# Optimization experiments

Hardware: AMD Instinct MI355X
Metric: run time of the kernel (lower is better)

The kernel has to match this reference:

```python
import jax, jax.numpy as jnp
import numpy as np

EPS = 1e-5
H = 1024  # hidden_size
IN = 1024  # input_size
B = 4096


def _layer_norm(x, gamma, beta):
    mu = jnp.mean(x, axis=-1, keepdims=True)
    var = jnp.mean(jnp.square(x - mu), axis=-1, keepdims=True)
    return (x - mu) * jax.lax.rsqrt(var + EPS) * gamma + beta


def setup_inputs() -> dict:
    key = jax.random.key(0)
    ks = jax.random.split(key, 8)
    s_h = 1.0 / np.sqrt(H)
    s_x = 1.0 / np.sqrt(IN)
    return {
        "x": jax.random.normal(ks[0], (B, IN), dtype=jnp.float32),
        "h": jax.random.normal(ks[1], (B, H), dtype=jnp.float32),
        "c": jax.random.normal(ks[2], (B, H), dtype=jnp.float32),
        # hidden_lin: Linear(H, 4H) with bias; input_lin: Linear(IN, 4H) no bias
        "W_h": jax.random.uniform(ks[3], (H, 4 * H), jnp.float32, -s_h, s_h),
        "b_h": jax.random.uniform(ks[4], (4 * H,), jnp.float32, -s_h, s_h),
        "W_x": jax.random.uniform(ks[5], (IN, 4 * H), jnp.float32, -s_x, s_x),
        # 4 gate LayerNorms stacked [4,H], plus LayerNorm for c
        "ln_g": jnp.ones((4, H), jnp.float32),
        "ln_b": jnp.zeros((4, H), jnp.float32),
        "lnc_g": jnp.ones((H,), jnp.float32),
        "lnc_b": jnp.zeros((H,), jnp.float32),
    }


def reference(x, h, c, W_h, b_h, W_x, ln_g, ln_b, lnc_g, lnc_b):
    # ifgo = hidden_lin(h) + input_lin(x) : [B, 4H]
    ifgo = h @ W_h + b_h + x @ W_x
    ifgo = ifgo.reshape(x.shape[0], 4, H)  # [B, 4, H]
    ifgo = _layer_norm(ifgo, ln_g, ln_b)   # per-gate LayerNorm over last dim
    i, f, g, o = ifgo[:, 0], ifgo[:, 1], ifgo[:, 2], ifgo[:, 3]
    c_next = jax.nn.sigmoid(f) * c + jax.nn.sigmoid(i) * jnp.tanh(g)
    h_next = jax.nn.sigmoid(o) * jnp.tanh(_layer_norm(c_next, lnc_g, lnc_b))
    return (h_next, c_next)
```

## Files before the change

kernel.cpp:

```cpp
#include <hip/hip_runtime.h>

typedef short bf16x8 __attribute__((ext_vector_type(8)));
typedef unsigned short u16x8 __attribute__((ext_vector_type(8)));
typedef float f32x4  __attribute__((ext_vector_type(4)));

__device__ __forceinline__ float bf2f(unsigned short u) {
  union { unsigned int i; float f; } x; x.i = ((unsigned int)u) << 16; return x.f;
}
__device__ __forceinline__ unsigned short f2bf(float f) {
  union { float f; unsigned int i; } x; x.f = f;
  unsigned int r = x.i + 0x7fffu + ((x.i >> 16) & 1u);
  return (unsigned short)(r >> 16);
}
__device__ __forceinline__ float sigm(float v) { return 1.f / (1.f + __expf(-v)); }
__device__ __forceinline__ float tanh_(float v) { return 1.f - 2.f / (__expf(2.f * v) + 1.f); }
__device__ __forceinline__ int is_fp32(const void* lng) {
  return ((*(const unsigned int*)lng) & 0xFFFFu) == 0u;
}

#define AS1 __attribute__((address_space(1)))
#define AS3 __attribute__((address_space(3)))

__global__ __launch_bounds__(256) void prep_kernel(
    const void* __restrict__ h, const void* __restrict__ x,
    const void* __restrict__ Wh, const void* __restrict__ Wx,
    const void* __restrict__ lng,
    unsigned short* __restrict__ Ap, unsigned short* __restrict__ Wt)
{
  __shared__ __align__(16) unsigned short tkn[64][64];
  const int fp = is_fp32(lng);
  if (blockIdx.x < 4096) {
    const int row = blockIdx.x;
    const int col = threadIdx.x * 8;
    const void* src; int sc;
    if (col < 1024) { src = h; sc = col; } else { src = x; sc = col - 1024; }
    u16x8 o;
    if (fp) {
      const float* s = (const float*)src + (size_t)row * 1024 + sc;
      float4 a = *(const float4*)s;
      float4 b = *(const float4*)(s + 4);
      o[0] = f2bf(a.x); o[1] = f2bf(a.y); o[2] = f2bf(a.z); o[3] = f2bf(a.w);
      o[4] = f2bf(b.x); o[5] = f2bf(b.y); o[6] = f2bf(b.z); o[7] = f2bf(b.w);
    } else {
      o = *(const u16x8*)((const unsigned short*)src + (size_t)row * 1024 + sc);
    }
    *(u16x8*)(Ap + (size_t)row * 2048 + col) = o;
  } else {
    const int bid = blockIdx.x - 4096;
    const int n0 = (bid & 63) * 64;
    const int k0 = (bid >> 6) * 64;
    const int t = threadIdx.x;
    const void* src; int krow;
    if (k0 < 1024) { src = Wh; krow = k0; } else { src = Wx; krow = k0 - 1024; }
    if (fp) {
#pragma unroll
      for (int i = 0; i < 4; ++i) {
        const int k  = (t >> 4) + i * 16;
        const int n4 = (t & 15) * 4;
        float4 w = *(const float4*)((const float*)src + (size_t)(krow + k) * 4096 + n0 + n4);
        ushort4 u; u.x = f2bf(w.x); u.y = f2bf(w.y); u.z = f2bf(w.z); u.w = f2bf(w.w);
        *(ushort4*)&tkn[k][n4] = u;
      }
    } else {
#pragma unroll
      for (int i = 0; i < 2; ++i) {
        const int k  = (t >> 3) + i * 32;
        const int n8 = (t & 7) * 8;
        *(u16x8*)&tkn[k][n8] =
            *(const u16x8*)((const unsigned short*)src + (size_t)(krow + k) * 4096 + n0 + n8);
      }
    }
    __syncthreads();
#pragma unroll
    for (int i = 0; i < 2; ++i) {
      const int n  = (t >> 3) + i * 32;
      const int k8 = (t & 7) * 8;
      u16x8 o;
#pragma unroll
      for (int j = 0; j < 8; ++j) o[j] = tkn[k8 + j][n];
      *(u16x8*)(Wt + (size_t)(n0 + n) * 2048 + k0 + k8) = o;
    }
  }
}


#define BAR()   __builtin_amdgcn_s_barrier()
#define VMW(N)  { asm volatile("s_waitcnt vmcnt(" #N ")" ::: "memory"); }
#define LGKM0() { asm volatile("s_waitcnt lgkmcnt(0)" ::: "memory"); }

#define LOAD_A(DB, MH)                                                         \
  { const unsigned short* _ba = &As[DB][(MH)*128 + wr*64 + fr][0];             \
    _Pragma("unroll") for (int mi = 0; mi < 4; ++mi)                           \
      _Pragma("unroll") for (int kh = 0; kh < 2; ++kh)                         \
        a[mi][kh] = *(const bf16x8*)(_ba + mi*1024 + ((kh*4 + fq) ^ xk) * 8); }

#define LOAD_B(DB, NH, BT)                                                     \
  { const unsigned short* _bb = &Bs[DB][(NH)*128 + wc*32 + fr][0];             \
    _Pragma("unroll") for (int ni = 0; ni < 2; ++ni)                           \
      _Pragma("unroll") for (int kh = 0; kh < 2; ++kh)                         \
        (BT)[ni][kh] = *(const bf16x8*)(_bb + ni*1024 + ((kh*4 + fq) ^ xk) * 8); }

#define MFMA16(MH, NH, BT)                                                     \
  { __builtin_amdgcn_s_setprio(1);                                             \
    _Pragma("unroll") for (int kh = 0; kh < 2; ++kh)                           \
      _Pragma("unroll") for (int mi = 0; mi < 4; ++mi)                         \
        _Pragma("unroll") for (int ni = 0; ni < 2; ++ni)                       \
          acc[MH][mi][NH][ni] = __builtin_amdgcn_mfma_f32_16x16x32_bf16(       \
              a[mi][kh], (BT)[ni][kh], acc[MH][mi][NH][ni], 0, 0, 0);          \
    __builtin_amdgcn_s_setprio(0); }

#define STAGE(G, LDS, ROW0, H, KT)                                             \
  { _Pragma("unroll") for (int l = 0; l < 2; ++l) {                            \
      const int _idx = l * 512 + tid;                                          \
      const int _r = _idx >> 3;                                                \
      const int _sg = (_idx & 7) ^ (_r & 7);                                   \
      const unsigned short* _src = (G) + (size_t)((ROW0) + (H)*128 + _r) * 2048\
                                   + ((KT) << 6) + _sg * 8;                    \
      __builtin_amdgcn_global_load_lds((const AS1 void*)_src,                  \
          (AS3 void*)(&(LDS)[0][0] + (H)*8192 + (l*512 + wave*64)*8), 16, 0, 0);\
  } }

__global__ __launch_bounds__(512, 2) void gemm_kernel(
    const unsigned short* __restrict__ Ap,
    const unsigned short* __restrict__ Wt,
    unsigned short* __restrict__ Cout)
{
  __shared__ __align__(16) unsigned short As[2][256][64];
  __shared__ __align__(16) unsigned short Bs[2][256][64];

  const int bid = blockIdx.x;
  const int swz = (bid & 7) * 32 + (bid >> 3);
  const int bm = swz >> 4, bn = swz & 15;
  const int arow = bm * 256, brow = bn * 256;

  const int tid  = threadIdx.x;
  const int wave = tid >> 6, lane = tid & 63;
  const int wr = wave >> 2, wc = wave & 3;
  const int fr = lane & 15, fq = lane >> 4;
  const int xk = fr & 7;

  f32x4 acc[2][4][2][2] = {};
  bf16x8 a[4][2], bA[2][2], bB[2][2];

  STAGE(Wt, Bs[0], brow, 0, 0);
  STAGE(Ap, As[0], arow, 0, 0);
  STAGE(Wt, Bs[0], brow, 1, 0);
  STAGE(Ap, As[0], arow, 1, 0);
  STAGE(Wt, Bs[1], brow, 0, 1);
  STAGE(Ap, As[1], arow, 0, 1);
  STAGE(Wt, Bs[1], brow, 1, 1);
  STAGE(Ap, As[1], arow, 1, 1);
  VMW(8);
  BAR();
  LOAD_B(0, 0, bA)
  LGKM0();

#pragma unroll 1
  for (int it = 0; it < 16; ++it) {
    const int t2 = (2 * it + 2) & 31;
    const int t3 = (2 * it + 3) & 31;

    LOAD_A(0, 0)
    STAGE(Wt, Bs[0], brow, 0, t2);
    BAR();
    MFMA16(0, 0, bA);
    BAR();
    LOAD_B(0, 1, bB)
    STAGE(Ap, As[0], arow, 0, t2);
    BAR();
    MFMA16(0, 1, bB);
    BAR();
    LOAD_A(0, 1)
    STAGE(Wt, Bs[0], brow, 1, t2);
    BAR();
    MFMA16(1, 1, bB);
    BAR();
    VMW(6);
    LOAD_B(1, 0, bB)
    STAGE(Ap, As[0], arow, 1, t2);
    BAR();
    MFMA16(1, 0, bA);
    LGKM0();
    BAR();
    LOAD_A(1, 0)
    STAGE(Wt, Bs[1], brow, 0, t3);
    BAR();
    MFMA16(0, 0, bB);
    BAR();
    LOAD_B(1, 1, bA)
    STAGE(Ap, As[1], arow, 0, t3);
    BAR();
    MFMA16(0, 1, bA);
    BAR();
    LOAD_A(1, 1)
    STAGE(Wt, Bs[1], brow, 1, t3);
    BAR();
    MFMA16(1, 1, bA);
    BAR();
    VMW(6);
    LOAD_B(0, 0, bA)
    STAGE(Ap, As[1], arow, 1, t3);
    BAR();
    MFMA16(1, 0, bB);
    LGKM0();
    BAR();
  }
  VMW(0);

  unsigned short* Cb = Cout + (size_t)arow * 4096 + brow;
#pragma unroll
  for (int mh = 0; mh < 2; ++mh)
#pragma unroll
    for (int mi = 0; mi < 4; ++mi)
#pragma unroll
      for (int nh = 0; nh < 2; ++nh)
#pragma unroll
        for (int ni = 0; ni < 2; ++ni) {
          const int row = mh * 128 + wr * 64 + mi * 16 + fq * 4;
          const int col = nh * 128 + wc * 32 + ni * 16 + fr;
#pragma unroll
          for (int r = 0; r < 4; ++r)
            Cb[(size_t)(row + r) * 4096 + col] = f2bf(acc[mh][mi][nh][ni][r]);
        }
}

__device__ __forceinline__ float4 load4(const void* p, size_t idx, int fp) {
  if (fp) return *(const float4*)((const float*)p + idx);
  ushort4 u = *(const ushort4*)((const unsigned short*)p + idx);
  return make_float4(bf2f(u.x), bf2f(u.y), bf2f(u.z), bf2f(u.w));
}
__device__ __forceinline__ void store4(void* p, size_t idx, int fp,
                                       float a, float b, float c, float d) {
  if (fp) {
    *(float4*)((float*)p + idx) = make_float4(a, b, c, d);
  } else {
    ushort4 u; u.x = f2bf(a); u.y = f2bf(b); u.z = f2bf(c); u.w = f2bf(d);
    *(ushort4*)((unsigned short*)p + idx) = u;
  }
}

__global__ __launch_bounds__(256) void ln_lstm_kernel(
    const unsigned short* __restrict__ parts,
    const void* __restrict__ c,
    const void* __restrict__ bh,
    const void* __restrict__ ln_g,
    const void* __restrict__ ln_b,
    const void* __restrict__ lnc_g,
    const void* __restrict__ lnc_b,
    void* __restrict__ out)
{
  const int t = threadIdx.x;
  const int lane = t & 63, wave = t >> 6;
  const int fp = is_fp32(lnc_g);

  __shared__ float sred[4][8];

  float4 bias4[4];
#pragma unroll
  for (int q = 0; q < 4; ++q) bias4[q] = load4(bh, q * 1024 + t * 4, fp);
  float gg[4][4], gb[4][4];
#pragma unroll
  for (int q = 0; q < 4; ++q) {
    float4 g4 = load4(ln_g, q * 1024 + t * 4, fp);
    float4 b4 = load4(ln_b, q * 1024 + t * 4, fp);
    gg[q][0] = g4.x; gg[q][1] = g4.y; gg[q][2] = g4.z; gg[q][3] = g4.w;
    gb[q][0] = b4.x; gb[q][1] = b4.y; gb[q][2] = b4.z; gb[q][3] = b4.w;
  }
  float4 cg4 = load4(lnc_g, t * 4, fp);
  float4 cb4 = load4(lnc_b, t * 4, fp);
  float cgv[4] = { cg4.x, cg4.y, cg4.z, cg4.w };
  float cbv[4] = { cb4.x, cb4.y, cb4.z, cb4.w };

#pragma unroll 1
  for (int r = 0; r < 4; ++r) {
    const int b = blockIdx.x * 4 + r;
    const unsigned short* P0 = parts + (size_t)b * 4096;
    __syncthreads();

    float v[4][4];
    float red[8];
#pragma unroll
    for (int q = 0; q < 4; ++q) {
      ushort4 p0 = *(const ushort4*)(P0 + q * 1024 + t * 4);
      v[q][0] = bf2f(p0.x) + bias4[q].x;
      v[q][1] = bf2f(p0.y) + bias4[q].y;
      v[q][2] = bf2f(p0.z) + bias4[q].z;
      v[q][3] = bf2f(p0.w) + bias4[q].w;
      red[q * 2]     = v[q][0] + v[q][1] + v[q][2] + v[q][3];
      red[q * 2 + 1] = v[q][0]*v[q][0] + v[q][1]*v[q][1] + v[q][2]*v[q][2] + v[q][3]*v[q][3];
    }
#pragma unroll
    for (int j = 0; j < 8; ++j) {
      float s = red[j];
#pragma unroll
      for (int off = 32; off > 0; off >>= 1) s += __shfl_down(s, off, 64);
      if (lane == 0) sred[wave][j] = s;
    }
    __syncthreads();
    float mu[4], rs[4];
#pragma unroll
    for (int q = 0; q < 4; ++q) {
      float s  = sred[0][2*q]   + sred[1][2*q]   + sred[2][2*q]   + sred[3][2*q];
      float sq = sred[0][2*q+1] + sred[1][2*q+1] + sred[2][2*q+1] + sred[3][2*q+1];
      mu[q] = s * (1.f / 1024.f);
      float var = sq * (1.f / 1024.f) - mu[q] * mu[q];
      rs[q] = rsqrtf(var + 1e-5f);
    }

    float4 c4 = load4(c, (size_t)b * 1024 + t * 4, fp);
    float cin[4] = { c4.x, c4.y, c4.z, c4.w };

    float cn[4], osg[4];
    float csum = 0.f, csq = 0.f;
#pragma unroll
    for (int e = 0; e < 4; ++e) {
      float iv = (v[0][e] - mu[0]) * rs[0] * gg[0][e] + gb[0][e];
      float fv = (v[1][e] - mu[1]) * rs[1] * gg[1][e] + gb[1][e];
      float gv = (v[2][e] - mu[2]) * rs[2] * gg[2][e] + gb[2][e];
      float ov = (v[3][e] - mu[3]) * rs[3] * gg[3][e] + gb[3][e];
      float cne = sigm(fv) * cin[e] + sigm(iv) * tanh_(gv);
      cn[e] = cne; csum += cne; csq += cne * cne;
      osg[e] = sigm(ov);
    }
    store4(out, (size_t)4096 * 1024 + (size_t)b * 1024 + t * 4, fp, cn[0], cn[1], cn[2], cn[3]);

    __syncthreads();
    {
      float s0 = csum, s1 = csq;
#pragma unroll
      for (int off = 32; off > 0; off >>= 1) { s0 += __shfl_down(s0, off, 64); s1 += __shfl_down(s1, off, 64); }
      if (lane == 0) { sred[wave][0] = s0; sred[wave][1] = s1; }
    }
    __syncthreads();
    float cs   = sred[0][0] + sred[1][0] + sred[2][0] + sred[3][0];
    float csq2 = sred[0][1] + sred[1][1] + sred[2][1] + sred[3][1];
    float mu_c = cs * (1.f / 1024.f);
    float var_c = csq2 * (1.f / 1024.f) - mu_c * mu_c;
    float rs_c = rsqrtf(var_c + 1e-5f);

    float hn[4];
#pragma unroll
    for (int e = 0; e < 4; ++e)
      hn[e] = osg[e] * tanh_((cn[e] - mu_c) * rs_c * cgv[e] + cbv[e]);
    store4(out, (size_t)b * 1024 + t * 4, fp, hn[0], hn[1], hn[2], hn[3]);
  }
}

extern "C" void kernel_launch(void* const* d_in, const int* in_sizes, int n_in,
                              void* d_out, int out_size, void* d_ws, size_t ws_size,
                              hipStream_t stream) {
  const void* x    = d_in[0];
  const void* h    = d_in[1];
  const void* c    = d_in[2];
  const void* Wh   = d_in[3];
  const void* bh   = d_in[4];
  const void* Wx   = d_in[5];
  const void* lng  = d_in[6];
  const void* lnb  = d_in[7];
  const void* lncg = d_in[8];
  const void* lncb = d_in[9];

  char* ws = (char*)d_ws;
  unsigned short* parts = (unsigned short*)ws;
  unsigned short* Wt    = (unsigned short*)(ws + (size_t)64 * 1024 * 1024);
  unsigned short* Ap    = (unsigned short*)(ws + (size_t)80 * 1024 * 1024);

  prep_kernel<<<6144, 256, 0, stream>>>(h, x, Wh, Wx, lng, Ap, Wt);
  gemm_kernel<<<256, 512, 0, stream>>>(Ap, Wt, parts);
  ln_lstm_kernel<<<1024, 256, 0, stream>>>(parts, c, bh, lng, lnb, lncg, lncb, d_out);
}
```

Baseline: 217.9 us.

## Fuse prep, GEMM and LayerNorm-LSTM into one persistent kernel with grid barriers

Merges the bf16 conversion/transpose prep kernel, the GEMM kernel and the LN-LSTM epilogue kernel into a single 256-block launch, separated by software grid-wide barriers built on atomic counters. Each block converts a slice of activations and weight tiles, syncs, runs the existing GEMM tile, syncs again, then does the LayerNorm/LSTM for 16 rows. The transpose scratch tile gains padding (stride 66) to reduce LDS bank conflicts. This removes launch gaps and tail effects between kernels, but needs all 256 blocks co-resident, adds a memset launch, and limits prep and epilogue parallelism to 256 blocks.

```diff
diff --git a/kernel.cpp b/kernel.cpp
--- a/kernel.cpp
+++ b/kernel.cpp
@@ -20,69 +20,6 @@
 
 #define AS1 __attribute__((address_space(1)))
 #define AS3 __attribute__((address_space(3)))
-
-__global__ __launch_bounds__(256) void prep_kernel(
-    const void* __restrict__ h, const void* __restrict__ x,
-    const void* __restrict__ Wh, const void* __restrict__ Wx,
-    const void* __restrict__ lng,
-    unsigned short* __restrict__ Ap, unsigned short* __restrict__ Wt)
-{
-  __shared__ __align__(16) unsigned short tkn[64][64];
-  const int fp = is_fp32(lng);
-  if (blockIdx.x < 4096) {
-    const int row = blockIdx.x;
-    const int col = threadIdx.x * 8;
-    const void* src; int sc;
-    if (col < 1024) { src = h; sc = col; } else { src = x; sc = col - 1024; }
-    u16x8 o;
-    if (fp) {
-      const float* s = (const float*)src + (size_t)row * 1024 + sc;
-      float4 a = *(const float4*)s;
-      float4 b = *(const float4*)(s + 4);
-      o[0] = f2bf(a.x); o[1] = f2bf(a.y); o[2] = f2bf(a.z); o[3] = f2bf(a.w);
-      o[4] = f2bf(b.x); o[5] = f2bf(b.y); o[6] = f2bf(b.z); o[7] = f2bf(b.w);
-    } else {
-      o = *(const u16x8*)((const unsigned short*)src + (size_t)row * 1024 + sc);
-    }
-    *(u16x8*)(Ap + (size_t)row * 2048 + col) = o;
-  } else {
-    const int bid = blockIdx.x - 4096;
-    const int n0 = (bid & 63) * 64;
-    const int k0 = (bid >> 6) * 64;
-    const int t = threadIdx.x;
-    const void* src; int krow;
-    if (k0 < 1024) { src = Wh; krow = k0; } else { src = Wx; krow = k0 - 1024; }
-    if (fp) {
-#pragma unroll
-      for (int i = 0; i < 4; ++i) {
-        const int k  = (t >> 4) + i * 16;
-        const int n4 = (t & 15) * 4;
-        float4 w = *(const float4*)((const float*)src + (size_t)(krow + k) * 4096 + n0 + n4);
-        ushort4 u; u.x = f2bf(w.x); u.y = f2bf(w.y); u.z = f2bf(w.z); u.w = f2bf(w.w);
-        *(ushort4*)&tkn[k][n4] = u;
-      }
-    } else {
-#pragma unroll
-      for (int i = 0; i < 2; ++i) {
-        const int k  = (t >> 3) + i * 32;
-        const int n8 = (t & 7) * 8;
-        *(u16x8*)&tkn[k][n8] =
-            *(const u16x8*)((const unsigned short*)src + (size_t)(krow + k) * 4096 + n0 + n8);
-      }
-    }
-    __syncthreads();
-#pragma unroll
-    for (int i = 0; i < 2; ++i) {
-      const int n  = (t >> 3) + i * 32;
-      const int k8 = (t & 7) * 8;
-      u16x8 o;
-#pragma unroll
-      for (int j = 0; j < 8; ++j) o[j] = tkn[k8 + j][n];
-      *(u16x8*)(Wt + (size_t)(n0 + n) * 2048 + k0 + k8) = o;
-    }
-  }
-}
-
 
 #define BAR()   __builtin_amdgcn_s_barrier()
 #define VMW(N)  { asm volatile("s_waitcnt vmcnt(" #N ")" ::: "memory"); }
@@ -120,229 +57,343 @@
           (AS3 void*)(&(LDS)[0][0] + (H)*8192 + (l*512 + wave*64)*8), 16, 0, 0);\
   } }
 
-__global__ __launch_bounds__(512, 2) void gemm_kernel(
-    const unsigned short* __restrict__ Ap,
-    const unsigned short* __restrict__ Wt,
-    unsigned short* __restrict__ Cout)
+__device__ __forceinline__ void grid_barrier(unsigned int* cnt, int tid) {
+  __threadfence();
+  __syncthreads();
+  if (tid == 0) {
+    atomicAdd(cnt, 1u);
+    int guard = 0;
+    while (atomicAdd(cnt, 0u) < 256u && guard < (1 << 20)) {
+      __builtin_amdgcn_s_sleep(8); ++guard;
+    }
+  }
+  __syncthreads();
+  __threadfence();
+}
+
+__global__ __launch_bounds__(512, 2) void fused_kernel(
+    const void* __restrict__ h, const void* __restrict__ x,
+    const void* __restrict__ Wh, const void* __restrict__ Wx,
+    const void* __restrict__ c,  const void* __restrict__ bh,
+    const void* __restrict__ ln_g, const void* __restrict__ ln_b,
+    const void* __restrict__ lnc_g, const void* __restrict__ lnc_b,
+    unsigned short* __restrict__ Ap, unsigned short* __restrict__ Wt,
+    unsigned short* __restrict__ parts, unsigned int* cnt,
+    void* __restrict__ out)
 {
   __shared__ __align__(16) unsigned short As[2][256][64];
   __shared__ __align__(16) unsigned short Bs[2][256][64];
+  __shared__ float sred[2][4][8];
 
   const int bid = blockIdx.x;
-  const int swz = (bid & 7) * 32 + (bid >> 3);
-  const int bm = swz >> 4, bn = swz & 15;
-  const int arow = bm * 256, brow = bn * 256;
-
-  const int tid  = threadIdx.x;
-  const int wave = tid >> 6, lane = tid & 63;
-  const int wr = wave >> 2, wc = wave & 3;
-  const int fr = lane & 15, fq = lane >> 4;
-  const int xk = fr & 7;
-
-  f32x4 acc[2][4][2][2] = {};
-  bf16x8 a[4][2], bA[2][2], bB[2][2];
-
-  STAGE(Wt, Bs[0], brow, 0, 0);
-  STAGE(Ap, As[0], arow, 0, 0);
-  STAGE(Wt, Bs[0], brow, 1, 0);
-  STAGE(Ap, As[0], arow, 1, 0);
-  STAGE(Wt, Bs[1], brow, 0, 1);
-  STAGE(Ap, As[1], arow, 0, 1);
-  STAGE(Wt, Bs[1], brow, 1, 1);
-  STAGE(Ap, As[1], arow, 1, 1);
-  VMW(8);
-  BAR();
-  LOAD_B(0, 0, bA)
-  LGKM0();
-
+  const int tid = threadIdx.x;
+  const int fp = is_fp32(ln_g);
+
+  {
+    const int team = tid >> 8, tt = tid & 255;
+#pragma unroll
+    for (int i = 0; i < 8; ++i) {
+      const int row = bid * 16 + i * 2 + team;
+      const int col = tt * 8;
+      const void* src; int sc;
+      if (col < 1024) { src = h; sc = col; } else { src = x; sc = col - 1024; }
+      u16x8 o;
+      if (fp) {
+        const float* s = (const float*)src + (size_t)row * 1024 + sc;
+        float4 a4 = *(const float4*)s;
+        float4 b4 = *(const float4*)(s + 4);
+        o[0] = f2bf(a4.x); o[1] = f2bf(a4.y); o[2] = f2bf(a4.z); o[3] = f2bf(a4.w);
+        o[4] = f2bf(b4.x); o[5] = f2bf(b4.y); o[6] = f2bf(b4.z); o[7] = f2bf(b4.w);
+      } else {
+        o = *(const u16x8*)((const unsigned short*)src + (size_t)row * 1024 + sc);
+      }
+      *(u16x8*)(Ap + (size_t)row * 2048 + col) = o;
+    }
+    unsigned short* tkn = ((unsigned short*)As) + team * (64 * 66);
 #pragma unroll 1
-  for (int it = 0; it < 16; ++it) {
-    const int t2 = (2 * it + 2) & 31;
-    const int t3 = (2 * it + 3) & 31;
-
-    LOAD_A(0, 0)
-    STAGE(Wt, Bs[0], brow, 0, t2);
+    for (int j = 0; j < 4; ++j) {
+      const int tile = bid * 8 + j * 2 + team;
+      const int n0 = (tile & 63) * 64;
+      const int k0 = (tile >> 6) * 64;
+      const void* src; int krow;
+      if (k0 < 1024) { src = Wh; krow = k0; } else { src = Wx; krow = k0 - 1024; }
+      __syncthreads();
+      if (fp) {
+#pragma unroll
+        for (int i = 0; i < 4; ++i) {
+          const int k  = (tt >> 4) + i * 16;
+          const int n4 = (tt & 15) * 4;
+          float4 w = *(const float4*)((const float*)src + (size_t)(krow + k) * 4096 + n0 + n4);
+          ushort2 u0; u0.x = f2bf(w.x); u0.y = f2bf(w.y);
+          ushort2 u1; u1.x = f2bf(w.z); u1.y = f2bf(w.w);
+          *(ushort2*)&tkn[k * 66 + n4]     = u0;
+          *(ushort2*)&tkn[k * 66 + n4 + 2] = u1;
+        }
+      } else {
+#pragma unroll
+        for (int i = 0; i < 2; ++i) {
+          const int k  = (tt >> 3) + i * 32;
+          const int n8 = (tt & 7) * 8;
+          u16x8 w = *(const u16x8*)((const unsigned short*)src + (size_t)(krow + k) * 4096 + n0 + n8);
+#pragma unroll
+          for (int q = 0; q < 4; ++q) {
+            ushort2 u; u.x = w[q * 2]; u.y = w[q * 2 + 1];
+            *(ushort2*)&tkn[k * 66 + n8 + q * 2] = u;
+          }
+        }
+      }
+      __syncthreads();
+#pragma unroll
+      for (int i = 0; i < 2; ++i) {
+        const int n  = (tt >> 3) + i * 32;
+        const int k8 = (tt & 7) * 8;
+        u16x8 o;
+#pragma unroll
+        for (int jj = 0; jj < 8; ++jj) o[jj] = tkn[(k8 + jj) * 66 + n];
+        *(u16x8*)(Wt + (size_t)(n0 + n) * 2048 + k0 + k8) = o;
+      }
+    }
+  }
+  grid_barrier(cnt, tid);
+
+  {
+    const int swz = (bid & 7) * 32 + (bid >> 3);
+    const int bm = swz >> 4, bn = swz & 15;
+    const int arow = bm * 256, brow = bn * 256;
+
+    const int wave = tid >> 6, lane = tid & 63;
+    const int wr = wave >> 2, wc = wave & 3;
+    const int fr = lane & 15, fq = lane >> 4;
+    const int xk = fr & 7;
+
+    f32x4 acc[2][4][2][2] = {};
+    bf16x8 a[4][2], bA[2][2], bB[2][2];
+
+    STAGE(Wt, Bs[0], brow, 0, 0);
+    STAGE(Ap, As[0], arow, 0, 0);
+    STAGE(Wt, Bs[0], brow, 1, 0);
+    STAGE(Ap, As[0], arow, 1, 0);
+    STAGE(Wt, Bs[1], brow, 0, 1);
+    STAGE(Ap, As[1], arow, 0, 1);
+    STAGE(Wt, Bs[1], brow, 1, 1);
+    STAGE(Ap, As[1], arow, 1, 1);
+    VMW(8);
     BAR();
-    MFMA16(0, 0, bA);
-    BAR();
-    LOAD_B(0, 1, bB)
-    STAGE(Ap, As[0], arow, 0, t2);
-    BAR();
-    MFMA16(0, 1, bB);
-    BAR();
-    LOAD_A(0, 1)
-    STAGE(Wt, Bs[0], brow, 1, t2);
-    BAR();
-    MFMA16(1, 1, bB);
-    BAR();
-    VMW(6);
-    LOAD_B(1, 0, bB)
-    STAGE(Ap, As[0], arow, 1, t2);
-    BAR();
-    MFMA16(1, 0, bA);
+    LOAD_B(0, 0, bA)
     LGKM0();
-    BAR();
-    LOAD_A(1, 0)
-    STAGE(Wt, Bs[1], brow, 0, t3);
-    BAR();
-    MFMA16(0, 0, bB);
-    BAR();
-    LOAD_B(1, 1, bA)
-    STAGE(Ap, As[1], arow, 0, t3);
-    BAR();
-    MFMA16(0, 1, bA);
-    BAR();
-    LOAD_A(1, 1)
-    STAGE(Wt, Bs[1], brow, 1, t3);
-    BAR();
-    MFMA16(1, 1, bA);
-    BAR();
-    VMW(6);
-    LOAD_B(0, 0, bA)
-    STAGE(Ap, As[1], arow, 1, t3);
-    BAR();
-    MFMA16(1, 0, bB);
-    LGKM0();
-    BAR();
+
+#pragma unroll 1
+    for (int it = 0; it < 16; ++it) {
+      const int t2 = (2 * it + 2) & 31;
+      const int t3 = (2 * it + 3) & 31;
+
+      LOAD_A(0, 0)
+      STAGE(Wt, Bs[0], brow, 0, t2);
+      BAR();
+      MFMA16(0, 0, bA);
+      BAR();
+
+      LOAD_B(0, 1, bB)
+      STAGE(Ap, As[0], arow, 0, t2);
+      BAR();
+      MFMA16(0, 1, bB);
+      BAR();
+
+      LOAD_A(0, 1)
+      STAGE(Wt, Bs[0], brow, 1, t2);
+      BAR();
+      MFMA16(1, 1, bB);
+      BAR();
+
+      VMW(6);
+      LOAD_B(1, 0, bB)
+      STAGE(Ap, As[0], arow, 1, t2);
+      BAR();
+      MFMA16(1, 0, bA);
+      LGKM0();
+      BAR();
+
+      LOAD_A(1, 0)
+      STAGE(Wt, Bs[1], brow, 0, t3);
+      BAR();
+      MFMA16(0, 0, bB);
+      BAR();
+
+      LOAD_B(1, 1, bA)
+      STAGE(Ap, As[1], arow, 0, t3);
+      BAR();
+      MFMA16(0, 1, bA);
+      BAR();
+
+      LOAD_A(1, 1)
+      STAGE(Wt, Bs[1], brow, 1, t3);
+      BAR();
+      MFMA16(1, 1, bA);
+      BAR();
+
+      VMW(6);
+      LOAD_B(0, 0, bA)
+      STAGE(Ap, As[1], arow, 1, t3);
+      BAR();
+      MFMA16(1, 0, bB);
+      LGKM0();
+      BAR();
+    }
+    VMW(0);
+
+    unsigned short* Cb = parts + (size_t)arow * 4096 + brow;
+#pragma unroll
+    for (int mh = 0; mh < 2; ++mh)
+#pragma unroll
+      for (int mi = 0; mi < 4; ++mi)
+#pragma unroll
+        for (int nh = 0; nh < 2; ++nh)
+#pragma unroll
+          for (int ni = 0; ni < 2; ++ni) {
+            const int row = mh * 128 + wr * 64 + mi * 16 + fq * 4;
+            const int col = nh * 128 + wc * 32 + ni * 16 + fr;
+#pragma unroll
+            for (int r = 0; r < 4; ++r)
+              Cb[(size_t)(row + r) * 4096 + col] = f2bf(acc[mh][mi][nh][ni][r]);
+          }
   }
-  VMW(0);
-
-  unsigned short* Cb = Cout + (size_t)arow * 4096 + brow;
-#pragma unroll
-  for (int mh = 0; mh < 2; ++mh)
-#pragma unroll
-    for (int mi = 0; mi < 4; ++mi)
-#pragma unroll
-      for (int nh = 0; nh < 2; ++nh)
-#pragma unroll
-        for (int ni = 0; ni < 2; ++ni) {
-          const int row = mh * 128 + wr * 64 + mi * 16 + fq * 4;
-          const int col = nh * 128 + wc * 32 + ni * 16 + fr;
-#pragma unroll
-          for (int r = 0; r < 4; ++r)
-            Cb[(size_t)(row + r) * 4096 + col] = f2bf(acc[mh][mi][nh][ni][r]);
-        }
-}
-
-__device__ __forceinline__ float4 load4(const void* p, size_t idx, int fp) {
-  if (fp) return *(const float4*)((const float*)p + idx);
-  ushort4 u = *(const ushort4*)((const unsigned short*)p + idx);
-  return make_float4(bf2f(u.x), bf2f(u.y), bf2f(u.z), bf2f(u.w));
-}
-__device__ __forceinline__ void store4(void* p, size_t idx, int fp,
-                                       float a, float b, float c, float d) {
-  if (fp) {
-    *(float4*)((float*)p + idx) = make_float4(a, b, c, d);
-  } else {
-    ushort4 u; u.x = f2bf(a); u.y = f2bf(b); u.z = f2bf(c); u.w = f2bf(d);
-    *(ushort4*)((unsigned short*)p + idx) = u;
-  }
-}
-
-__global__ __launch_bounds__(256) void ln_lstm_kernel(
-    const unsigned short* __restrict__ parts,
-    const void* __restrict__ c,
-    const void* __restrict__ bh,
-    const void* __restrict__ ln_g,
-    const void* __restrict__ ln_b,
-    const void* __restrict__ lnc_g,
-    const void* __restrict__ lnc_b,
-    void* __restrict__ out)
-{
-  const int t = threadIdx.x;
-  const int lane = t & 63, wave = t >> 6;
-  const int fp = is_fp32(lnc_g);
-
-  __shared__ float sred[4][8];
-
-  float4 bias4[4];
-#pragma unroll
-  for (int q = 0; q < 4; ++q) bias4[q] = load4(bh, q * 1024 + t * 4, fp);
-  float gg[4][4], gb[4][4];
-#pragma unroll
-  for (int q = 0; q < 4; ++q) {
-    float4 g4 = load4(ln_g, q * 1024 + t * 4, fp);
-    float4 b4 = load4(ln_b, q * 1024 + t * 4, fp);
-    gg[q][0] = g4.x; gg[q][1] = g4.y; gg[q][2] = g4.z; gg[q][3] = g4.w;
-    gb[q][0] = b4.x; gb[q][1] = b4.y; gb[q][2] = b4.z; gb[q][3] = b4.w;
-  }
-  float4 cg4 = load4(lnc_g, t * 4, fp);
-  float4 cb4 = load4(lnc_b, t * 4, fp);
-  float cgv[4] = { cg4.x, cg4.y, cg4.z, cg4.w };
-  float cbv[4] = { cb4.x, cb4.y, cb4.z, cb4.w };
+  grid_barrier(cnt + 16, tid);
+
+  {
+    const int team = tid >> 8, tt = tid & 255;
+    const int lane = tt & 63, wave4 = tt >> 6;
+
+    float4 bias4[4];
+#pragma unroll
+    for (int q = 0; q < 4; ++q) {
+      if (fp) bias4[q] = *(const float4*)((const float*)bh + q * 1024 + tt * 4);
+      else {
+        ushort4 u = *(const ushort4*)((const unsigned short*)bh + q * 1024 + tt * 4);
+        bias4[q] = make_float4(bf2f(u.x), bf2f(u.y), bf2f(u.z), bf2f(u.w));
+      }
+    }
+    float gg[4][4], gb[4][4];
+#pragma unroll
+    for (int q = 0; q < 4; ++q) {
+      float4 g4, b4;
+      if (fp) {
+        g4 = *(const float4*)((const float*)ln_g + q * 1024 + tt * 4);
+        b4 = *(const float4*)((const float*)ln_b + q * 1024 + tt * 4);
+      } else {
+        ushort4 ug = *(const ushort4*)((const unsigned short*)ln_g + q * 1024 + tt * 4);
+        ushort4 ub = *(const ushort4*)((const unsigned short*)ln_b + q * 1024 + tt * 4);
+        g4 = make_float4(bf2f(ug.x), bf2f(ug.y), bf2f(ug.z), bf2f(ug.w));
+        b4 = make_float4(bf2f(ub.x), bf2f(ub.y), bf2f(ub.z), bf2f(ub.w));
+      }
+      gg[q][0] = g4.x; gg[q][1] = g4.y; gg[q][2] = g4.z; gg[q][3] = g4.w;
+      gb[q][0] = b4.x; gb[q][1] = b4.y; gb[q][2] = b4.z; gb[q][3] = b4.w;
+    }
+    float cgv[4], cbv[4];
+    {
+      float4 g4, b4;
+      if (fp) {
+        g4 = *(const float4*)((const float*)lnc_g + tt * 4);
+        b4 = *(const float4*)((const float*)lnc_b + tt * 4);
+      } else {
+        ushort4 ug = *(const ushort4*)((const unsigned short*)lnc_g + tt * 4);
+        ushort4 ub = *(const ushort4*)((const unsigned short*)lnc_b + tt * 4);
+        g4 = make_float4(bf2f(ug.x), bf2f(ug.y), bf2f(ug.z), bf2f(ug.w));
+        b4 = make_float4(bf2f(ub.x), bf2f(ub.y), bf2f(ub.z), bf2f(ub.w));
+      }
+      cgv[0] = g4.x; cgv[1] = g4.y; cgv[2] = g4.z; cgv[3] = g4.w;
+      cbv[0] = b4.x; cbv[1] = b4.y; cbv[2] = b4.z; cbv[3] = b4.w;
+    }
 
 #pragma unroll 1
-  for (int r = 0; r < 4; ++r) {
-    const int b = blockIdx.x * 4 + r;
-    const unsigned short* P0 = parts + (size_t)b * 4096;
-    __syncthreads();
-
-    float v[4][4];
-    float red[8];
-#pragma unroll
-    for (int q = 0; q < 4; ++q) {
-      ushort4 p0 = *(const ushort4*)(P0 + q * 1024 + t * 4);
-      v[q][0] = bf2f(p0.x) + bias4[q].x;
-      v[q][1] = bf2f(p0.y) + bias4[q].y;
-      v[q][2] = bf2f(p0.z) + bias4[q].z;
-      v[q][3] = bf2f(p0.w) + bias4[q].w;
-      red[q * 2]     = v[q][0] + v[q][1] + v[q][2] + v[q][3];
-      red[q * 2 + 1] = v[q][0]*v[q][0] + v[q][1]*v[q][1] + v[q][2]*v[q][2] + v[q][3]*v[q][3];
-    }
-#pragma unroll
-    for (int j = 0; j < 8; ++j) {
-      float s = red[j];
-#pragma unroll
-      for (int off = 32; off > 0; off >>= 1) s += __shfl_down(s, off, 64);
-      if (lane == 0) sred[wave][j] = s;
-    }
-    __syncthreads();
-    float mu[4], rs[4];
-#pragma unroll
-    for (int q = 0; q < 4; ++q) {
-      float s  = sred[0][2*q]   + sred[1][2*q]   + sred[2][2*q]   + sred[3][2*q];
-      float sq = sred[0][2*q+1] + sred[1][2*q+1] + sred[2][2*q+1] + sred[3][2*q+1];
-      mu[q] = s * (1.f / 1024.f);
-      float var = sq * (1.f / 1024.f) - mu[q] * mu[q];
-      rs[q] = rsqrtf(var + 1e-5f);
-    }
-
-    float4 c4 = load4(c, (size_t)b * 1024 + t * 4, fp);
-    float cin[4] = { c4.x, c4.y, c4.z, c4.w };
-
-    float cn[4], osg[4];
-    float csum = 0.f, csq = 0.f;
-#pragma unroll
-    for (int e = 0; e < 4; ++e) {
-      float iv = (v[0][e] - mu[0]) * rs[0] * gg[0][e] + gb[0][e];
-      float fv = (v[1][e] - mu[1]) * rs[1] * gg[1][e] + gb[1][e];
-      float gv = (v[2][e] - mu[2]) * rs[2] * gg[2][e] + gb[2][e];
-      float ov = (v[3][e] - mu[3]) * rs[3] * gg[3][e] + gb[3][e];
-      float cne = sigm(fv) * cin[e] + sigm(iv) * tanh_(gv);
-      cn[e] = cne; csum += cne; csq += cne * cne;
-      osg[e] = sigm(ov);
-    }
-    store4(out, (size_t)4096 * 1024 + (size_t)b * 1024 + t * 4, fp, cn[0], cn[1], cn[2], cn[3]);
-
-    __syncthreads();
-    {
-      float s0 = csum, s1 = csq;
-#pragma unroll
-      for (int off = 32; off > 0; off >>= 1) { s0 += __shfl_down(s0, off, 64); s1 += __shfl_down(s1, off, 64); }
-      if (lane == 0) { sred[wave][0] = s0; sred[wave][1] = s1; }
-    }
-    __syncthreads();
-    float cs   = sred[0][0] + sred[1][0] + sred[2][0] + sred[3][0];
-    float csq2 = sred[0][1] + sred[1][1] + sred[2][1] + sred[3][1];
-    float mu_c = cs * (1.f / 1024.f);
-    float var_c = csq2 * (1.f / 1024.f) - mu_c * mu_c;
-    float rs_c = rsqrtf(var_c + 1e-5f);
-
-    float hn[4];
-#pragma unroll
-    for (int e = 0; e < 4; ++e)
-      hn[e] = osg[e] * tanh_((cn[e] - mu_c) * rs_c * cgv[e] + cbv[e]);
-    store4(out, (size_t)b * 1024 + t * 4, fp, hn[0], hn[1], hn[2], hn[3]);
+    for (int r = 0; r < 8; ++r) {
+      const int b = bid * 16 + team * 8 + r;
+      const unsigned short* P0 = parts + (size_t)b * 4096;
+      __syncthreads();
+
+      float v[4][4];
+      float red[8];
+#pragma unroll
+      for (int q = 0; q < 4; ++q) {
+        ushort4 p0 = *(const ushort4*)(P0 + q * 1024 + tt * 4);
+        v[q][0] = bf2f(p0.x) + bias4[q].x;
+        v[q][1] = bf2f(p0.y) + bias4[q].y;
+        v[q][2] = bf2f(p0.z) + bias4[q].z;
+        v[q][3] = bf2f(p0.w) + bias4[q].w;
+        red[q * 2]     = v[q][0] + v[q][1] + v[q][2] + v[q][3];
+        red[q * 2 + 1] = v[q][0]*v[q][0] + v[q][1]*v[q][1] + v[q][2]*v[q][2] + v[q][3]*v[q][3];
+      }
+#pragma unroll
+      for (int j = 0; j < 8; ++j) {
+        float s = red[j];
+#pragma unroll
+        for (int off = 32; off > 0; off >>= 1) s += __shfl_down(s, off, 64);
+        if (lane == 0) sred[team][wave4][j] = s;
+      }
+      __syncthreads();
+      float mu[4], rs[4];
+#pragma unroll
+      for (int q = 0; q < 4; ++q) {
+        float s  = sred[team][0][2*q]   + sred[team][1][2*q]   + sred[team][2][2*q]   + sred[team][3][2*q];
+        float sq = sred[team][0][2*q+1] + sred[team][1][2*q+1] + sred[team][2][2*q+1] + sred[team][3][2*q+1];
+        mu[q] = s * (1.f / 1024.f);
+        float var = sq * (1.f / 1024.f) - mu[q] * mu[q];
+        rs[q] = rsqrtf(var + 1e-5f);
+      }
+
+      float4 c4;
+      if (fp) c4 = *(const float4*)((const float*)c + (size_t)b * 1024 + tt * 4);
+      else {
+        ushort4 u = *(const ushort4*)((const unsigned short*)c + (size_t)b * 1024 + tt * 4);
+        c4 = make_float4(bf2f(u.x), bf2f(u.y), bf2f(u.z), bf2f(u.w));
+      }
+      float cin[4] = { c4.x, c4.y, c4.z, c4.w };
+
+      float cn[4], osg[4];
+      float csum = 0.f, csq = 0.f;
+#pragma unroll
+      for (int e = 0; e < 4; ++e) {
+        float iv = (v[0][e] - mu[0]) * rs[0] * gg[0][e] + gb[0][e];
+        float fv = (v[1][e] - mu[1]) * rs[1] * gg[1][e] + gb[1][e];
+        float gv = (v[2][e] - mu[2]) * rs[2] * gg[2][e] + gb[2][e];
+        float ov = (v[3][e] - mu[3]) * rs[3] * gg[3][e] + gb[3][e];
+        float cne = sigm(fv) * cin[e] + sigm(iv) * tanh_(gv);
+        cn[e] = cne; csum += cne; csq += cne * cne;
+        osg[e] = sigm(ov);
+      }
+      if (fp) {
+        *(float4*)((float*)out + (size_t)4096 * 1024 + (size_t)b * 1024 + tt * 4) =
+            make_float4(cn[0], cn[1], cn[2], cn[3]);
+      } else {
+        ushort4 u; u.x = f2bf(cn[0]); u.y = f2bf(cn[1]); u.z = f2bf(cn[2]); u.w = f2bf(cn[3]);
+        *(ushort4*)((unsigned short*)out + (size_t)4096 * 1024 + (size_t)b * 1024 + tt * 4) = u;
+      }
+
+      __syncthreads();
+      {
+        float s0 = csum, s1 = csq;
+#pragma unroll
+        for (int off = 32; off > 0; off >>= 1) { s0 += __shfl_down(s0, off, 64); s1 += __shfl_down(s1, off, 64); }
+        if (lane == 0) { sred[team][wave4][0] = s0; sred[team][wave4][1] = s1; }
+      }
+      __syncthreads();
+      float cs   = sred[team][0][0] + sred[team][1][0] + sred[team][2][0] + sred[team][3][0];
+      float csq2 = sred[team][0][1] + sred[team][1][1] + sred[team][2][1] + sred[team][3][1];
+      float mu_c = cs * (1.f / 1024.f);
+      float var_c = csq2 * (1.f / 1024.f) - mu_c * mu_c;
+      float rs_c = rsqrtf(var_c + 1e-5f);
+
+      float hn[4];
+#pragma unroll
+      for (int e = 0; e < 4; ++e)
+        hn[e] = osg[e] * tanh_((cn[e] - mu_c) * rs_c * cgv[e] + cbv[e]);
+      if (fp) {
+        *(float4*)((float*)out + (size_t)b * 1024 + tt * 4) =
+            make_float4(hn[0], hn[1], hn[2], hn[3]);
+      } else {
+        ushort4 u; u.x = f2bf(hn[0]); u.y = f2bf(hn[1]); u.z = f2bf(hn[2]); u.w = f2bf(hn[3]);
+        *(ushort4*)((unsigned short*)out + (size_t)b * 1024 + tt * 4) = u;
+      }
+    }
   }
 }
 
@@ -362,10 +413,11 @@
 
   char* ws = (char*)d_ws;
   unsigned short* parts = (unsigned short*)ws;
+  unsigned int*   cnt   = (unsigned int*)(ws + (size_t)48 * 1024 * 1024);
   unsigned short* Wt    = (unsigned short*)(ws + (size_t)64 * 1024 * 1024);
   unsigned short* Ap    = (unsigned short*)(ws + (size_t)80 * 1024 * 1024);
 
-  prep_kernel<<<6144, 256, 0, stream>>>(h, x, Wh, Wx, lng, Ap, Wt);
-  gemm_kernel<<<256, 512, 0, stream>>>(Ap, Wt, parts);
-  ln_lstm_kernel<<<1024, 256, 0, stream>>>(parts, c, bh, lng, lnb, lncg, lncb, d_out);
-}
+  hipMemsetAsync(cnt, 0, 256, stream);
+  fused_kernel<<<256, 512, 0, stream>>>(h, x, Wh, Wx, c, bh, lng, lnb, lncg, lncb,
+                                        Ap, Wt, parts, cnt, d_out);
+}
```

Result: slower. 452.1 us (+107.5%).
